# Optimization experiments

Hardware: AMD Instinct MI355X
Metric: run time of the kernel (lower is better)

The kernel has to match this reference:

```python
import jax, jax.numpy as jnp
import numpy as np

B, N, D = 4, 4096, 256

def setup_inputs() -> dict:
    key = jax.random.key(0)
    k1, = jax.random.split(key, 1)
    x = jax.random.normal(k1, (B, N, D), dtype=jnp.float32)
    attn_mask = jnp.ones((B, 1, N), dtype=jnp.int32)
    pad_mask = jnp.ones((B, 1, N), dtype=jnp.int32)
    return {"x": x, "attn_mask": attn_mask, "pad_mask": pad_mask, "dim_": D}

def reference(x, attn_mask, pad_mask, dim_):
    # adj is None -> scores = x @ x^T / sqrt(d)
    scale = jnp.sqrt(jnp.asarray(x.shape[-1], x.dtype))
    scores = jnp.einsum('bnd,bmd->bnm', x, x) / scale  # [B, N, N]
    # NOTE: original calls non-in-place masked_fill and discards the result,
    # so pad_mask / attn_mask have no effect on the output (faithful).
    prob = jax.nn.softmax(scores, axis=-1)
    # dropout is identity in inference mode
    return jnp.einsum('bnm,bmd->bnd', prob, x)
```

## Files before the change

### kernel.cpp

```cpp
#include <hip/hip_runtime.h>

typedef __attribute__((ext_vector_type(8))) short short8;
typedef __attribute__((ext_vector_type(4))) float f32x4;
typedef __attribute__((ext_vector_type(4))) unsigned int u32x4;

#define NTOK 4096
#define DIM  256
#define P_STRIDE 72
#define TILE_ELEMS 32768

__device__ __forceinline__ unsigned pack2bf(float a, float b) {
  unsigned ua = __builtin_bit_cast(unsigned, a) + 0x8000u;
  unsigned ub = __builtin_bit_cast(unsigned, b) + 0x8000u;
  return __builtin_amdgcn_perm(ub, ua, 0x07060302u);
}

__global__ __launch_bounds__(256, 4)
void prep_kernel(const float* __restrict__ X, unsigned short* __restrict__ Img) {
  const int b    = blockIdx.x & 3;
  const int sub  = blockIdx.x >> 2;
  const int t    = sub >> 3;
  const int part = sub & 7;
  const int tid  = threadIdx.x;
  const float* src = X + ((size_t)b * NTOK + t * 64) * DIM;
  unsigned short* dst = Img + ((size_t)(b * 64 + t)) * TILE_ELEMS;
  {
    int r = part * 8 + (tid >> 5);
    int c = tid & 31;
    const float* s = src + r * DIM + c * 8;
    f32x4 f0 = *(const f32x4*)s;
    f32x4 f1 = *(const f32x4*)(s + 4);
    union { unsigned u[4]; u32x4 v; } p;
    p.u[0] = pack2bf(f0[0], f0[1]);
    p.u[1] = pack2bf(f0[2], f0[3]);
    p.u[2] = pack2bf(f1[0], f1[1]);
    p.u[3] = pack2bf(f1[2], f1[3]);
    *(u32x4*)(dst + r * 256 + ((c ^ (r & 7)) << 3)) = p.v;
  }
  {
    const int d = tid;
    float f[8];
    #pragma unroll
    for (int i = 0; i < 8; ++i) f[i] = src[(part * 8 + i) * DIM + d];
    union { unsigned u[4]; u32x4 v; } p;
    p.u[0] = pack2bf(f[0], f[1]);
    p.u[1] = pack2bf(f[2], f[3]);
    p.u[2] = pack2bf(f[4], f[5]);
    p.u[3] = pack2bf(f[6], f[7]);
    *(u32x4*)(dst + 16384 + part * 2048 + d * 8) = p.v;
  }
}

__device__ __forceinline__ void pv_step(const unsigned short* __restrict__ pr,
                                        const unsigned short* __restrict__ kt,
                                        f32x4 (&o)[2][4],
                                        int qh, int role, int quad, int ln) {
  #pragma unroll
  for (int ks = 0; ks < 2; ++ks) {
    const int pos = (ks * 4 + quad) ^ ((ln >> 3) << 1);
    short8 ap[2], bv[4];
    #pragma unroll
    for (int s = 0; s < 2; ++s) {
      const int r = qh * 32 + s * 16 + ln;
      ap[s] = *(const short8*)(&pr[r * P_STRIDE + (pos << 3)]);
    }
    const unsigned short* kb = kt + (ks * 4 + quad) * 2048 + (role * 64 + ln) * 8;
    #pragma unroll
    for (int dt = 0; dt < 4; ++dt) bv[dt] = *(const short8*)(kb + dt * 128);
    #pragma unroll
    for (int s = 0; s < 2; ++s)
      #pragma unroll
      for (int dt = 0; dt < 4; ++dt)
        o[s][dt] = __builtin_amdgcn_mfma_f32_16x16x32_bf16(ap[s], bv[dt], o[s][dt], 0, 0, 0);
  }
}

__global__ __launch_bounds__(512, 1)
void fa_kernel(const unsigned short* __restrict__ Img, float* __restrict__ Out) {
  __shared__ __align__(16) unsigned short ksb[2][16384];
  __shared__ __align__(16) unsigned short ktb[2][16384];
  __shared__ __align__(16) unsigned short pb[2][64 * P_STRIDE];
  __shared__ float lbuf[64][4];

  const int tid  = threadIdx.x;
  const int b    = blockIdx.x & 3;
  const int qblk = blockIdx.x >> 2;
  const int wave = tid >> 6;
  const int lane = tid & 63;
  const int ln   = lane & 15;
  const int quad = lane >> 4;
  const int swz  = ln & 7;
  const int qh   = wave & 1;
  const int role = wave >> 1;

  const unsigned short* imgb  = Img + (size_t)b * 64 * TILE_ELEMS;
  const char*           imgbc = (const char*)imgb;

  short8 aQ[2][8];
  #pragma unroll
  for (int s = 0; s < 2; ++s) {
    const unsigned short* qrow =
        imgb + (size_t)qblk * TILE_ELEMS + (qh * 32 + s * 16 + ln) * 256;
    #pragma unroll
    for (int ds = 0; ds < 8; ++ds)
      aQ[s][ds] = *(const short8*)(qrow + (((ds * 4 + quad) ^ swz) << 3));
  }

  f32x4 o[2][4];
  #pragma unroll
  for (int s = 0; s < 2; ++s)
    #pragma unroll
    for (int dt = 0; dt < 4; ++dt) o[s][dt] = (f32x4)(0.0f);
  float lrow[2][4] = {{0.f,0.f,0.f,0.f},{0.f,0.f,0.f,0.f}};

  const float c2 = 0.0901684400f;

  const int pwPos = ((role * 2 + (ln >> 3)) ^ ((quad >> 1) << 1)) << 3;
  const int pwCol = ln & 7;

  const bool dmaKs = wave < 4;
  const int  dmaQ  = wave & 3;
  const char* gK = imgbc + (size_t)dmaQ * 8192 + (size_t)lane * 16;

  if (dmaKs) {
    #pragma unroll
    for (int i = 0; i < 8; ++i)
      __builtin_amdgcn_global_load_lds(
          (const __attribute__((address_space(1))) unsigned*)(gK + i * 1024),
          (__attribute__((address_space(3))) unsigned*)(&ksb[0][dmaQ * 4096 + i * 512]),
          16, 0, 0);
  }

  for (int t = 0; t < 64; ++t) {
    __syncthreads();
    const int buf = t & 1;

    if (dmaKs) {
      if (t < 63) {
        const char* g = gK + (size_t)(t + 1) * 65536;
        unsigned short* l = &ksb[buf ^ 1][dmaQ * 4096];
        #pragma unroll
        for (int i = 0; i < 8; ++i)
          __builtin_amdgcn_global_load_lds(
              (const __attribute__((address_space(1))) unsigned*)(g + i * 1024),
              (__attribute__((address_space(3))) unsigned*)(l + i * 512),
              16, 0, 0);
      }
    } else {
      const char* g = gK + (size_t)t * 65536 + 32768;
      unsigned short* l = &ktb[buf][dmaQ * 4096];
      #pragma unroll
      for (int i = 0; i < 8; ++i)
        __builtin_amdgcn_global_load_lds(
            (const __attribute__((address_space(1))) unsigned*)(g + i * 1024),
            (__attribute__((address_space(3))) unsigned*)(l + i * 512),
            16, 0, 0);
    }

    f32x4 sf0 = (f32x4)(0.0f), sf1 = (f32x4)(0.0f);
    {
      const unsigned short* krow = &ksb[buf][(role * 16 + ln) * 256];
      #pragma unroll
      for (int ds = 0; ds < 8; ++ds) {
        short8 bk = *(const short8*)(krow + (((ds * 4 + quad) ^ swz) << 3));
        sf0 = __builtin_amdgcn_mfma_f32_16x16x32_bf16(aQ[0][ds], bk, sf0, 0, 0, 0);
        sf1 = __builtin_amdgcn_mfma_f32_16x16x32_bf16(aQ[1][ds], bk, sf1, 0, 0, 0);
      }
    }
    {
      unsigned short* pw = pb[buf];
      #pragma unroll
      for (int j = 0; j < 4; ++j) {
        float p0 = __builtin_amdgcn_exp2f(sf0[j] * c2);
        float p1 = __builtin_amdgcn_exp2f(sf1[j] * c2);
        lrow[0][j] += p0;
        lrow[1][j] += p1;
        unsigned q0 = __builtin_bit_cast(unsigned, p0);
        unsigned q1 = __builtin_bit_cast(unsigned, p1);
        unsigned n0 = (unsigned)__builtin_amdgcn_mov_dpp((int)q0, 0xB1, 0xF, 0xF, true);
        unsigned n1 = (unsigned)__builtin_amdgcn_mov_dpp((int)q1, 0xB1, 0xF, 0xF, true);
        if ((ln & 1) == 0) {
          const int r0 = qh * 32 + quad * 4 + j;
          unsigned d0 = pack2bf(__builtin_bit_cast(float, q0), __builtin_bit_cast(float, n0));
          unsigned d1 = pack2bf(__builtin_bit_cast(float, q1), __builtin_bit_cast(float, n1));
          *(unsigned*)(&pw[r0 * P_STRIDE + pwPos + pwCol]) = d0;
          *(unsigned*)(&pw[(r0 + 16) * P_STRIDE + pwPos + pwCol]) = d1;
        }
      }
    }

    if (t > 0)
      pv_step(pb[buf ^ 1], ktb[buf ^ 1], o, qh, role, quad, ln);
  }

  __syncthreads();
  pv_step(pb[1], ktb[1], o, qh, role, quad, ln);

  #pragma unroll
  for (int off = 1; off < 16; off <<= 1)
    #pragma unroll
    for (int s = 0; s < 2; ++s)
      #pragma unroll
      for (int j = 0; j < 4; ++j)
        lrow[s][j] += __shfl_xor(lrow[s][j], off, 64);
  if (ln == 0) {
    #pragma unroll
    for (int s = 0; s < 2; ++s)
      #pragma unroll
      for (int j = 0; j < 4; ++j)
        lbuf[qh * 32 + s * 16 + quad * 4 + j][role] = lrow[s][j];
  }
  __syncthreads();

  #pragma unroll
  for (int s = 0; s < 2; ++s) {
    float* outp = Out + (size_t)(b * NTOK + qblk * 64 + qh * 32 + s * 16) * DIM + role * 64;
    #pragma unroll
    for (int j = 0; j < 4; ++j) {
      const int row = s * 16 + quad * 4 + j;
      f32x4 lv = *(const f32x4*)lbuf[qh * 32 + row];
      const float rl = 1.0f / (lv[0] + lv[1] + lv[2] + lv[3]);
      #pragma unroll
      for (int dt = 0; dt < 4; ++dt)
        outp[(size_t)(quad * 4 + j) * DIM + dt * 16 + ln] = o[s][dt][j] * rl;
    }
  }
}

extern "C" void kernel_launch(void* const* d_in, const int* in_sizes, int n_in,
                              void* d_out, int out_size, void* d_ws, size_t ws_size,
                              hipStream_t stream) {
  const float* X = (const float*)d_in[0];
  float* Out = (float*)d_out;
  unsigned short* Img = (unsigned short*)d_ws;
  (void)in_sizes; (void)n_in; (void)out_size; (void)ws_size;
  hipLaunchKernelGGL(prep_kernel, dim3(2048), dim3(256), 0, stream, X, Img);
  hipLaunchKernelGGL(fa_kernel, dim3(256), dim3(512), 0, stream, Img, Out);
}
```

Baseline: 173.5 us.

## Load K operand directly into registers instead of staging through LDS

```diff
diff --git a/kernel.cpp b/kernel.cpp
--- a/kernel.cpp
+++ b/kernel.cpp
@@ -7,7 +7,8 @@
 #define NTOK 4096
 #define DIM  256
 #define P_STRIDE 72
-#define TILE_ELEMS 32768
+#define XBF_ELEMS (4u * NTOK * DIM)
+#define KT_TILE 16384
 
 __device__ __forceinline__ unsigned pack2bf(float a, float b) {
   unsigned ua = __builtin_bit_cast(unsigned, a) + 0x8000u;
@@ -16,14 +17,15 @@
 }
 
 __global__ __launch_bounds__(256, 4)
-void prep_kernel(const float* __restrict__ X, unsigned short* __restrict__ Img) {
+void prep_kernel(const float* __restrict__ X, unsigned short* __restrict__ Ws) {
+  unsigned short* Xbf = Ws;
+  unsigned short* Kti = Ws + XBF_ELEMS;
   const int b    = blockIdx.x & 3;
   const int sub  = blockIdx.x >> 2;
   const int t    = sub >> 3;
   const int part = sub & 7;
   const int tid  = threadIdx.x;
   const float* src = X + ((size_t)b * NTOK + t * 64) * DIM;
-  unsigned short* dst = Img + ((size_t)(b * 64 + t)) * TILE_ELEMS;
   {
     int r = part * 8 + (tid >> 5);
     int c = tid & 31;
@@ -35,7 +37,7 @@
     p.u[1] = pack2bf(f0[2], f0[3]);
     p.u[2] = pack2bf(f1[0], f1[1]);
     p.u[3] = pack2bf(f1[2], f1[3]);
-    *(u32x4*)(dst + r * 256 + ((c ^ (r & 7)) << 3)) = p.v;
+    *(u32x4*)(Xbf + ((size_t)b * NTOK + t * 64 + r) * DIM + c * 8) = p.v;
   }
   {
     const int d = tid;
@@ -47,7 +49,7 @@
     p.u[1] = pack2bf(f[2], f[3]);
     p.u[2] = pack2bf(f[4], f[5]);
     p.u[3] = pack2bf(f[6], f[7]);
-    *(u32x4*)(dst + 16384 + part * 2048 + d * 8) = p.v;
+    *(u32x4*)(Kti + ((size_t)(b * 64 + t)) * KT_TILE + part * 2048 + d * 8) = p.v;
   }
 }
 
@@ -76,11 +78,13 @@
 }
 
 __global__ __launch_bounds__(512, 1)
-void fa_kernel(const unsigned short* __restrict__ Img, float* __restrict__ Out) {
-  __shared__ __align__(16) unsigned short ksb[2][16384];
-  __shared__ __align__(16) unsigned short ktb[2][16384];
+void fa_kernel(const unsigned short* __restrict__ Ws, float* __restrict__ Out) {
+  __shared__ __align__(16) unsigned short ktb[2][KT_TILE];
   __shared__ __align__(16) unsigned short pb[2][64 * P_STRIDE];
   __shared__ float lbuf[64][4];
+
+  const unsigned short* Xbf = Ws;
+  const unsigned short* Kti = Ws + XBF_ELEMS;
 
   const int tid  = threadIdx.x;
   const int b    = blockIdx.x & 3;
@@ -89,21 +93,18 @@
   const int lane = tid & 63;
   const int ln   = lane & 15;
   const int quad = lane >> 4;
-  const int swz  = ln & 7;
   const int qh   = wave & 1;
   const int role = wave >> 1;
 
-  const unsigned short* imgb  = Img + (size_t)b * 64 * TILE_ELEMS;
-  const char*           imgbc = (const char*)imgb;
+  const unsigned short* xb = Xbf + (size_t)b * NTOK * DIM;
 
   short8 aQ[2][8];
   #pragma unroll
   for (int s = 0; s < 2; ++s) {
-    const unsigned short* qrow =
-        imgb + (size_t)qblk * TILE_ELEMS + (qh * 32 + s * 16 + ln) * 256;
+    const unsigned short* qrow = xb + (size_t)(qblk * 64 + qh * 32 + s * 16 + ln) * DIM + quad * 8;
     #pragma unroll
     for (int ds = 0; ds < 8; ++ds)
-      aQ[s][ds] = *(const short8*)(qrow + (((ds * 4 + quad) ^ swz) << 3));
+      aQ[s][ds] = *(const short8*)(qrow + ds * 32);
   }
 
   f32x4 o[2][4];
@@ -118,39 +119,24 @@
   const int pwPos = ((role * 2 + (ln >> 3)) ^ ((quad >> 1) << 1)) << 3;
   const int pwCol = ln & 7;
 
-  const bool dmaKs = wave < 4;
-  const int  dmaQ  = wave & 3;
-  const char* gK = imgbc + (size_t)dmaQ * 8192 + (size_t)lane * 16;
-
-  if (dmaKs) {
-    #pragma unroll
-    for (int i = 0; i < 8; ++i)
-      __builtin_amdgcn_global_load_lds(
-          (const __attribute__((address_space(1))) unsigned*)(gK + i * 1024),
-          (__attribute__((address_space(3))) unsigned*)(&ksb[0][dmaQ * 4096 + i * 512]),
-          16, 0, 0);
-  }
+  const char* gKt = (const char*)(Kti + (size_t)b * 64 * KT_TILE) +
+                    (size_t)wave * 4096 + (size_t)lane * 16;
+
+  const unsigned short* kstream = xb + (size_t)(role * 16 + ln) * DIM + quad * 8;
+  short8 bk[8];
+  #pragma unroll
+  for (int ds = 0; ds < 8; ++ds)
+    bk[ds] = *(const short8*)(kstream + ds * 32);
 
   for (int t = 0; t < 64; ++t) {
     __syncthreads();
     const int buf = t & 1;
 
-    if (dmaKs) {
-      if (t < 63) {
-        const char* g = gK + (size_t)(t + 1) * 65536;
-        unsigned short* l = &ksb[buf ^ 1][dmaQ * 4096];
-        #pragma unroll
-        for (int i = 0; i < 8; ++i)
-          __builtin_amdgcn_global_load_lds(
-              (const __attribute__((address_space(1))) unsigned*)(g + i * 1024),
-              (__attribute__((address_space(3))) unsigned*)(l + i * 512),
-              16, 0, 0);
-      }
-    } else {
-      const char* g = gK + (size_t)t * 65536 + 32768;
-      unsigned short* l = &ktb[buf][dmaQ * 4096];
-      #pragma unroll
-      for (int i = 0; i < 8; ++i)
+    {
+      const char* g = gKt + (size_t)t * 32768;
+      unsigned short* l = &ktb[buf][wave * 2048];
+      #pragma unroll
+      for (int i = 0; i < 4; ++i)
         __builtin_amdgcn_global_load_lds(
             (const __attribute__((address_space(1))) unsigned*)(g + i * 1024),
             (__attribute__((address_space(3))) unsigned*)(l + i * 512),
@@ -158,15 +144,19 @@
     }
 
     f32x4 sf0 = (f32x4)(0.0f), sf1 = (f32x4)(0.0f);
-    {
-      const unsigned short* krow = &ksb[buf][(role * 16 + ln) * 256];
-      #pragma unroll
-      for (int ds = 0; ds < 8; ++ds) {
-        short8 bk = *(const short8*)(krow + (((ds * 4 + quad) ^ swz) << 3));
-        sf0 = __builtin_amdgcn_mfma_f32_16x16x32_bf16(aQ[0][ds], bk, sf0, 0, 0, 0);
-        sf1 = __builtin_amdgcn_mfma_f32_16x16x32_bf16(aQ[1][ds], bk, sf1, 0, 0, 0);
-      }
-    }
+    #pragma unroll
+    for (int ds = 0; ds < 8; ++ds) {
+      sf0 = __builtin_amdgcn_mfma_f32_16x16x32_bf16(aQ[0][ds], bk[ds], sf0, 0, 0, 0);
+      sf1 = __builtin_amdgcn_mfma_f32_16x16x32_bf16(aQ[1][ds], bk[ds], sf1, 0, 0, 0);
+    }
+
+    if (t < 63) {
+      const unsigned short* kr = kstream + (size_t)(t + 1) * 64 * DIM;
+      #pragma unroll
+      for (int ds = 0; ds < 8; ++ds)
+        bk[ds] = *(const short8*)(kr + ds * 32);
+    }
+
     {
       unsigned short* pw = pb[buf];
       #pragma unroll
@@ -232,8 +222,8 @@
                               hipStream_t stream) {
   const float* X = (const float*)d_in[0];
   float* Out = (float*)d_out;
-  unsigned short* Img = (unsigned short*)d_ws;
+  unsigned short* Ws = (unsigned short*)d_ws;
   (void)in_sizes; (void)n_in; (void)out_size; (void)ws_size;
-  hipLaunchKernelGGL(prep_kernel, dim3(2048), dim3(256), 0, stream, X, Img);
-  hipLaunchKernelGGL(fa_kernel, dim3(256), dim3(512), 0, stream, Img, Out);
-}
+  hipLaunchKernelGGL(prep_kernel, dim3(2048), dim3(256), 0, stream, X, Ws);
+  hipLaunchKernelGGL(fa_kernel, dim3(256), dim3(512), 0, stream, Ws, Out);
+}
```

Result: slower. 249.4 us (+43.8%).

## Fuse bf16 prep into attention kernel with grid-wide atomic barrier

Applied to the files above, without the earlier changes.

```diff
diff --git a/kernel.cpp b/kernel.cpp
--- a/kernel.cpp
+++ b/kernel.cpp
@@ -8,6 +8,7 @@
 #define DIM  256
 #define P_STRIDE 72
 #define TILE_ELEMS 32768
+#define CNT_OFF (16u * 1024u * 1024u)
 
 __device__ __forceinline__ unsigned pack2bf(float a, float b) {
   unsigned ua = __builtin_bit_cast(unsigned, a) + 0x8000u;
@@ -15,56 +16,18 @@
   return __builtin_amdgcn_perm(ub, ua, 0x07060302u);
 }
 
-__global__ __launch_bounds__(256, 4)
-void prep_kernel(const float* __restrict__ X, unsigned short* __restrict__ Img) {
-  const int b    = blockIdx.x & 3;
-  const int sub  = blockIdx.x >> 2;
-  const int t    = sub >> 3;
-  const int part = sub & 7;
-  const int tid  = threadIdx.x;
-  const float* src = X + ((size_t)b * NTOK + t * 64) * DIM;
-  unsigned short* dst = Img + ((size_t)(b * 64 + t)) * TILE_ELEMS;
-  {
-    int r = part * 8 + (tid >> 5);
-    int c = tid & 31;
-    const float* s = src + r * DIM + c * 8;
-    f32x4 f0 = *(const f32x4*)s;
-    f32x4 f1 = *(const f32x4*)(s + 4);
-    union { unsigned u[4]; u32x4 v; } p;
-    p.u[0] = pack2bf(f0[0], f0[1]);
-    p.u[1] = pack2bf(f0[2], f0[3]);
-    p.u[2] = pack2bf(f1[0], f1[1]);
-    p.u[3] = pack2bf(f1[2], f1[3]);
-    *(u32x4*)(dst + r * 256 + ((c ^ (r & 7)) << 3)) = p.v;
-  }
-  {
-    const int d = tid;
-    float f[8];
-    #pragma unroll
-    for (int i = 0; i < 8; ++i) f[i] = src[(part * 8 + i) * DIM + d];
-    union { unsigned u[4]; u32x4 v; } p;
-    p.u[0] = pack2bf(f[0], f[1]);
-    p.u[1] = pack2bf(f[2], f[3]);
-    p.u[2] = pack2bf(f[4], f[5]);
-    p.u[3] = pack2bf(f[6], f[7]);
-    *(u32x4*)(dst + 16384 + part * 2048 + d * 8) = p.v;
-  }
-}
-
 __device__ __forceinline__ void pv_step(const unsigned short* __restrict__ pr,
                                         const unsigned short* __restrict__ kt,
                                         f32x4 (&o)[2][4],
-                                        int qh, int role, int quad, int ln) {
+                                        int qh, int dq, int quad, int ln) {
   #pragma unroll
   for (int ks = 0; ks < 2; ++ks) {
     const int pos = (ks * 4 + quad) ^ ((ln >> 3) << 1);
     short8 ap[2], bv[4];
     #pragma unroll
-    for (int s = 0; s < 2; ++s) {
-      const int r = qh * 32 + s * 16 + ln;
-      ap[s] = *(const short8*)(&pr[r * P_STRIDE + (pos << 3)]);
-    }
-    const unsigned short* kb = kt + (ks * 4 + quad) * 2048 + (role * 64 + ln) * 8;
+    for (int s = 0; s < 2; ++s)
+      ap[s] = *(const short8*)(&pr[(qh * 32 + s * 16 + ln) * P_STRIDE + (pos << 3)]);
+    const unsigned short* kb = kt + (ks * 4 + quad) * 2048 + (dq * 64 + ln) * 8;
     #pragma unroll
     for (int dt = 0; dt < 4; ++dt) bv[dt] = *(const short8*)(kb + dt * 128);
     #pragma unroll
@@ -76,7 +39,8 @@
 }
 
 __global__ __launch_bounds__(512, 1)
-void fa_kernel(const unsigned short* __restrict__ Img, float* __restrict__ Out) {
+void fa_kernel(const float* __restrict__ X, unsigned short* __restrict__ Img,
+               int* __restrict__ cnt, float* __restrict__ Out) {
   __shared__ __align__(16) unsigned short ksb[2][16384];
   __shared__ __align__(16) unsigned short ktb[2][16384];
   __shared__ __align__(16) unsigned short pb[2][64 * P_STRIDE];
@@ -93,6 +57,49 @@
   const int qh   = wave & 1;
   const int role = wave >> 1;
 
+  {
+    const float* src = X + ((size_t)b * NTOK + qblk * 64) * DIM;
+    unsigned short* dst = Img + (size_t)(b * 64 + qblk) * TILE_ELEMS;
+    #pragma unroll
+    for (int i = 0; i < 4; ++i) {
+      int c   = i * 512 + tid;
+      int r   = c >> 5;
+      int cc  = c & 31;
+      const float* s = src + r * DIM + cc * 8;
+      f32x4 f0 = *(const f32x4*)s;
+      f32x4 f1 = *(const f32x4*)(s + 4);
+      union { unsigned u[4]; u32x4 v; } p;
+      p.u[0] = pack2bf(f0[0], f0[1]);
+      p.u[1] = pack2bf(f0[2], f0[3]);
+      p.u[2] = pack2bf(f1[0], f1[1]);
+      p.u[3] = pack2bf(f1[2], f1[3]);
+      *(u32x4*)(dst + r * 256 + ((cc ^ (r & 7)) << 3)) = p.v;
+    }
+    if (tid < 256) {
+      const int d = tid;
+      #pragma unroll
+      for (int kb = 0; kb < 8; ++kb) {
+        float f[8];
+        #pragma unroll
+        for (int i = 0; i < 8; ++i) f[i] = src[(kb * 8 + i) * DIM + d];
+        union { unsigned u[4]; u32x4 v; } p;
+        p.u[0] = pack2bf(f[0], f[1]);
+        p.u[1] = pack2bf(f[2], f[3]);
+        p.u[2] = pack2bf(f[4], f[5]);
+        p.u[3] = pack2bf(f[6], f[7]);
+        *(u32x4*)(dst + 16384 + kb * 2048 + d * 8) = p.v;
+      }
+    }
+  }
+
+  __syncthreads();
+  if (tid == 0) {
+    __hip_atomic_fetch_add(cnt, 1, __ATOMIC_RELEASE, __HIP_MEMORY_SCOPE_AGENT);
+    while (__hip_atomic_load(cnt, __ATOMIC_ACQUIRE, __HIP_MEMORY_SCOPE_AGENT) < 256)
+      __builtin_amdgcn_s_sleep(8);
+  }
+  __syncthreads();
+
   const unsigned short* imgb  = Img + (size_t)b * 64 * TILE_ELEMS;
   const char*           imgbc = (const char*)imgb;
 
@@ -114,7 +121,6 @@
   float lrow[2][4] = {{0.f,0.f,0.f,0.f},{0.f,0.f,0.f,0.f}};
 
   const float c2 = 0.0901684400f;
-
   const int pwPos = ((role * 2 + (ln >> 3)) ^ ((quad >> 1) << 1)) << 3;
   const int pwCol = ln & 7;
 
@@ -233,7 +239,8 @@
   const float* X = (const float*)d_in[0];
   float* Out = (float*)d_out;
   unsigned short* Img = (unsigned short*)d_ws;
+  int* cnt = (int*)((char*)d_ws + CNT_OFF);
   (void)in_sizes; (void)n_in; (void)out_size; (void)ws_size;
-  hipLaunchKernelGGL(prep_kernel, dim3(2048), dim3(256), 0, stream, X, Img);
-  hipLaunchKernelGGL(fa_kernel, dim3(256), dim3(512), 0, stream, Img, Out);
-}
+  hipMemsetAsync(cnt, 0, 4, stream);
+  hipLaunchKernelGGL(fa_kernel, dim3(256), dim3(512), 0, stream, X, Img, cnt, Out);
+}
```

Measured after the change: 194.6 us. 1.12x slower.
